# Kernel optimization log

Hardware: AMD Instinct MI355X
Metric: run time of the kernel (lower is better)

The kernel has to match this reference:

```python
import jax, jax.numpy as jnp
import numpy as np

N = 100000      # nodes
E = 1600000     # graph edges (avg degree 16)
Q = 1000000     # query edges to score
IN, HID, OUT = 128, 128, 64


def setup_inputs() -> dict:
    key = jax.random.key(0)
    ks = jax.random.split(key, 7)
    feat = jax.random.normal(ks[0], (N, IN), dtype=jnp.float32)
    edge_src = jax.random.randint(ks[1], (E,), 0, N, dtype=jnp.int32)
    edge_dst = jax.random.randint(ks[2], (E,), 0, N, dtype=jnp.int32)
    src = jax.random.randint(ks[3], (Q,), 0, N, dtype=jnp.int32)
    dst = jax.random.randint(ks[4], (Q,), 0, N, dtype=jnp.int32)
    W1 = jax.random.normal(ks[5], (IN, HID), dtype=jnp.float32) / np.sqrt(IN).astype(np.float32)
    b1 = jnp.zeros((HID,), jnp.float32)
    W2 = jax.random.normal(ks[6], (HID, OUT), dtype=jnp.float32) / np.sqrt(HID).astype(np.float32)
    b2 = jnp.zeros((OUT,), jnp.float32)
    return {"feat": feat, "edge_src": edge_src, "edge_dst": edge_dst,
            "src": src, "dst": dst, "W1": W1, "b1": b1, "W2": W2, "b2": b2}


def _graph_conv(h, W, b, edge_src, edge_dst, out_norm, in_norm):
    """DGL GraphConv(norm='both'): D_out^{-1/2} -> aggregate -> D_in^{-1/2}, W, b.
    DGL applies W before aggregation when in_feats > out_feats (same math)."""
    n = h.shape[0]
    h = h * out_norm[:, None]
    if h.shape[1] > W.shape[1]:
        h = h @ W
        agg = jax.ops.segment_sum(h[edge_src], edge_dst, num_segments=n)
    else:
        agg = jax.ops.segment_sum(h[edge_src], edge_dst, num_segments=n)
        agg = agg @ W
    return agg * in_norm[:, None] + b


def reference(feat, edge_src, edge_dst, src, dst, W1, b1, W2, b2):
    n = feat.shape[0]
    ones = jnp.ones((edge_src.shape[0],), feat.dtype)
    out_deg = jax.ops.segment_sum(ones, edge_src, num_segments=n)
    in_deg = jax.ops.segment_sum(ones, edge_dst, num_segments=n)
    out_norm = jnp.maximum(out_deg, 1.0) ** -0.5
    in_norm = jnp.maximum(in_deg, 1.0) ** -0.5

    h = _graph_conv(feat, W1, b1, edge_src, edge_dst, out_norm, in_norm)
    h = jax.nn.relu(h)  # dropout is identity at inference
    h = _graph_conv(h, W2, b2, edge_src, edge_dst, out_norm, in_norm)

    edge_scores = jnp.sum(h[src] * h[dst], axis=-1)
    return jax.nn.sigmoid(edge_scores)
```

## Files before the change

kernel.cpp:

```cpp
#include <hip/hip_runtime.h>
#include <math.h>

static inline size_t align256(size_t x) { return (x + 255) & ~(size_t)255; }

typedef __attribute__((ext_vector_type(8))) short bf16x8;
typedef __attribute__((ext_vector_type(4))) float f32x4;

__device__ inline float bfLo(unsigned int u) {
  union { unsigned int i; float f; } v; v.i = u << 16; return v.f;
}
__device__ inline float bfHi(unsigned int u) {
  union { unsigned int i; float f; } v; v.i = u & 0xffff0000u; return v.f;
}
__device__ inline float bf2f(unsigned short u) {
  union { unsigned int i; float f; } v; v.i = ((unsigned int)u) << 16; return v.f;
}
__device__ inline unsigned short f2bf(float f) {
  union { float f; unsigned int i; } v; v.f = f;
  unsigned int r = v.i + 0x7FFF + ((v.i >> 16) & 1);
  return (unsigned short)(r >> 16);
}
__device__ inline unsigned int packbf(float lo, float hi) {
  return ((unsigned int)f2bf(hi) << 16) | f2bf(lo);
}

__global__ __launch_bounds__(256) void k_coarse_count(const int* __restrict__ esrc,
                                                      const int* __restrict__ edst,
                                                      int E, int chunk, int NB, int G,
                                                      int* __restrict__ blkD,
                                                      int* __restrict__ blkS) {
  __shared__ int hD[512], hS[512];
  int blk = blockIdx.x, tid = threadIdx.x;
  for (int i = tid; i < NB; i += 256) { hD[i] = 0; hS[i] = 0; }
  __syncthreads();
  int s0 = blk * chunk, s1 = min(E, s0 + chunk);
  for (int e = s0 + tid; e < s1; e += 256) {
    atomicAdd(&hD[edst[e] >> 8], 1);
    atomicAdd(&hS[esrc[e] >> 8], 1);
  }
  __syncthreads();
  for (int i = tid; i < NB; i += 256) {
    blkD[i * G + blk] = hD[i];
    blkS[i * G + blk] = hS[i];
  }
}

__global__ __launch_bounds__(256) void k_scan1(const int* __restrict__ in,
                                               int* __restrict__ out,
                                               int* __restrict__ bsums, int n) {
  __shared__ int s[256];
  int tid = threadIdx.x, gid = blockIdx.x * 256 + tid;
  int v = (gid < n) ? in[gid] : 0;
  s[tid] = v; __syncthreads();
  for (int o = 1; o < 256; o <<= 1) {
    int t = (tid >= o) ? s[tid - o] : 0;
    __syncthreads();
    s[tid] += t;
    __syncthreads();
  }
  if (gid < n) out[gid] = s[tid] - v;
  if (tid == 255) bsums[blockIdx.x] = s[255];
}

__global__ __launch_bounds__(512) void k_scan2(int* __restrict__ bsums, int nb) {
  __shared__ int s[512];
  int tid = threadIdx.x;
  int* base = bsums + blockIdx.x * nb;
  int v = (tid < nb) ? base[tid] : 0;
  s[tid] = v; __syncthreads();
  for (int o = 1; o < 512; o <<= 1) {
    int t = (tid >= o) ? s[tid - o] : 0;
    __syncthreads();
    s[tid] += t;
    __syncthreads();
  }
  if (tid < nb) base[tid] = s[tid] - v;
}

__global__ __launch_bounds__(256) void k_scan3b(int* __restrict__ arr,
                                                const int* __restrict__ bsums, int n) {
  int gid = blockIdx.x * 256 + threadIdx.x;
  if (gid < n) arr[gid] += bsums[blockIdx.x];
}

__global__ __launch_bounds__(256) void k_coarse_scatter(const int* __restrict__ esrc,
                                                        const int* __restrict__ edst,
                                                        int E, int chunk, int NB, int G,
                                                        const int* __restrict__ scD,
                                                        const int* __restrict__ scS,
                                                        unsigned int* __restrict__ pairs,
                                                        unsigned int* __restrict__ keys) {
  __shared__ int cD[512], cS[512];
  int blk = blockIdx.x, tid = threadIdx.x;
  for (int i = tid; i < NB; i += 256) {
    cD[i] = scD[i * G + blk];
    cS[i] = scS[i * G + blk];
  }
  __syncthreads();
  int s0 = blk * chunk, s1 = min(E, s0 + chunk);
  for (int e = s0 + tid; e < s1; e += 256) {
    int s = esrc[e], d = edst[e];
    int pd = atomicAdd(&cD[d >> 8], 1);
    pairs[pd] = ((unsigned)s << 8) | ((unsigned)d & 255u);
    int ps = atomicAdd(&cS[s >> 8], 1);
    keys[ps] = (unsigned)s;
  }
}

__global__ __launch_bounds__(256) void k_fine(const unsigned int* __restrict__ pairs,
                                              const unsigned int* __restrict__ keys,
                                              const int* __restrict__ scD,
                                              const int* __restrict__ scS,
                                              int G, int E, int N, int NB,
                                              int* __restrict__ cntIn,
                                              float* __restrict__ normIn,
                                              int* __restrict__ offs,
                                              int* __restrict__ csr,
                                              float* __restrict__ normOut) {
  __shared__ int hist[256], scn[256], cur[256];
  int tid = threadIdx.x;
  if (blockIdx.x >= (unsigned)NB) {
    int b = blockIdx.x - NB;
    int bstart = scS[b * G];
    int bend = (b + 1 < NB) ? scS[(b + 1) * G] : E;
    hist[tid] = 0;
    __syncthreads();
    for (int e = bstart + tid; e < bend; e += 256)
      atomicAdd(&hist[keys[e] & 255u], 1);
    __syncthreads();
    int node = b * 256 + tid;
    if (node < N) normOut[node] = rsqrtf((float)max(hist[tid], 1));
    return;
  }
  int b = blockIdx.x;
  int bstart = scD[b * G];
  int bend = (b + 1 < NB) ? scD[(b + 1) * G] : E;
  hist[tid] = 0;
  __syncthreads();
  for (int e = bstart + tid; e < bend; e += 256)
    atomicAdd(&hist[pairs[e] & 255u], 1);
  __syncthreads();
  int v = hist[tid];
  scn[tid] = v;
  __syncthreads();
  for (int o = 1; o < 256; o <<= 1) {
    int t = (tid >= o) ? scn[tid - o] : 0;
    __syncthreads();
    scn[tid] += t;
    __syncthreads();
  }
  int excl = scn[tid] - v;
  cur[tid] = excl;
  int node = b * 256 + tid;
  if (node < N) {
    cntIn[node] = v;
    normIn[node] = rsqrtf((float)max(v, 1));
    offs[node] = bstart + excl;
  }
  __syncthreads();
  for (int e = bstart + tid; e < bend; e += 256) {
    unsigned int u = pairs[e];
    int p = bstart + atomicAdd(&cur[u & 255u], 1);
    csr[p] = (int)(u >> 8);
  }
}

__global__ __launch_bounds__(256) void k_prep(const float* __restrict__ W1,
                                              const float* __restrict__ W2,
                                              unsigned short* __restrict__ W1t,
                                              unsigned short* __restrict__ W2t) {
  int t = blockIdx.x * 256 + threadIdx.x;
  int stride = gridDim.x * 256;
  for (int i = t; i < 128 * 128; i += stride) {
    int nn = i >> 7, kk = i & 127;
    W1t[i] = f2bf(W1[kk * 128 + nn]);
  }
  for (int i = t; i < 64 * 128; i += stride) {
    int nn = i >> 7, kk = i & 127;
    W2t[i] = f2bf(W2[kk * 64 + nn]);
  }
}

template <int C, typename TA>
__global__ __launch_bounds__(256) void k_mgemm(const TA* __restrict__ A,
                                               const float* __restrict__ scale,
                                               const unsigned short* __restrict__ Wt,
                                               unsigned short* __restrict__ out, int n) {
  constexpr int KP = 136;
  constexpr int NCH = C / 16;
  __shared__ __align__(16) unsigned short Al[64 * KP];
  __shared__ __align__(16) unsigned short Wl[C * KP];
  int tid = threadIdx.x;
  int r0 = blockIdx.x * 64;

  {
    const uint4* Wg = (const uint4*)Wt;
    uint4* Wd = (uint4*)Wl;
    for (int idx = tid; idx < C * 16; idx += 256) {
      int row = idx >> 4, seg = idx & 15;
      Wd[row * 17 + seg] = Wg[idx];
    }
  }
  {
    int seg = tid & 7;
    for (int it = 0; it < 2; ++it) {
      int row = (tid >> 3) + it * 32;
      int g = r0 + row;
      float v[16];
      if (g < n) {
        float sc = scale[g];
        if constexpr (sizeof(TA) == 4) {
          const float4* Ag = (const float4*)((const float*)A + (size_t)g * 128);
#pragma unroll
          for (int j = 0; j < 4; ++j) {
            float4 f = Ag[seg * 4 + j];
            v[j * 4 + 0] = f.x * sc; v[j * 4 + 1] = f.y * sc;
            v[j * 4 + 2] = f.z * sc; v[j * 4 + 3] = f.w * sc;
          }
        } else {
          const uint4* Ag = (const uint4*)((const unsigned short*)A + (size_t)g * 128);
#pragma unroll
          for (int j = 0; j < 2; ++j) {
            uint4 u = Ag[seg * 2 + j];
            v[j * 8 + 0] = bfLo(u.x) * sc; v[j * 8 + 1] = bfHi(u.x) * sc;
            v[j * 8 + 2] = bfLo(u.y) * sc; v[j * 8 + 3] = bfHi(u.y) * sc;
            v[j * 8 + 4] = bfLo(u.z) * sc; v[j * 8 + 5] = bfHi(u.z) * sc;
            v[j * 8 + 6] = bfLo(u.w) * sc; v[j * 8 + 7] = bfHi(u.w) * sc;
          }
        }
      } else {
#pragma unroll
        for (int j = 0; j < 16; ++j) v[j] = 0.f;
      }
      uint4* dst = (uint4*)(Al + row * KP + seg * 16);
      dst[0] = make_uint4(packbf(v[0], v[1]), packbf(v[2], v[3]),
                          packbf(v[4], v[5]), packbf(v[6], v[7]));
      dst[1] = make_uint4(packbf(v[8], v[9]), packbf(v[10], v[11]),
                          packbf(v[12], v[13]), packbf(v[14], v[15]));
    }
  }
  __syncthreads();

  int lane = tid & 63;
  int w = tid >> 6;
  int quad = lane >> 4, m16 = lane & 15;
  f32x4 acc[NCH];
#pragma unroll
  for (int c = 0; c < NCH; ++c) acc[c] = (f32x4){0.f, 0.f, 0.f, 0.f};

#pragma unroll
  for (int kc = 0; kc < 4; ++kc) {
    int ko = kc * 32 + quad * 8;
    bf16x8 a = *(const bf16x8*)(Al + (w * 16 + m16) * KP + ko);
#pragma unroll
    for (int c = 0; c < NCH; ++c) {
      bf16x8 b = *(const bf16x8*)(Wl + (c * 16 + m16) * KP + ko);
      acc[c] = __builtin_amdgcn_mfma_f32_16x16x32_bf16(a, b, acc[c], 0, 0, 0);
    }
  }

#pragma unroll
  for (int c = 0; c < NCH; ++c)
#pragma unroll
    for (int r = 0; r < 4; ++r) {
      int g = r0 + w * 16 + quad * 4 + r;
      if (g < n) out[(size_t)g * C + c * 16 + m16] = f2bf(acc[c][r]);
    }
}

__global__ __launch_bounds__(256) void k_agg128_relu(const unsigned short* __restrict__ X,
                                                     const int* __restrict__ csr,
                                                     const int* __restrict__ offs,
                                                     const int* __restrict__ cnt,
                                                     const float* __restrict__ norm,
                                                     const float* __restrict__ bias,
                                                     unsigned short* __restrict__ H, int n) {
  int wid = blockIdx.x * 4 + (threadIdx.x >> 6);
  if (wid >= n) return;
  int lane = threadIdx.x & 63;
  int sub = lane & 15;
  int grp = lane >> 4;
  int start = offs[wid], m = cnt[wid];
  const int* p = csr + start;
  const uint4* Xv = (const uint4*)X;
  float a[8] = {0.f, 0.f, 0.f, 0.f, 0.f, 0.f, 0.f, 0.f};
  for (int c0 = 0; c0 < m; c0 += 64) {
    int take = min(64, m - c0);
    int iv = p[c0 + ((lane < take) ? lane : take - 1)];
    int e = 0;
    for (; e + 16 <= take; e += 16) {
      uint4 uu[4];
#pragma unroll
      for (int j = 0; j < 4; ++j) {
        int ss = __shfl(iv, e + j * 4 + grp);
        uu[j] = Xv[(size_t)ss * 16 + sub];
      }
#pragma unroll
      for (int j = 0; j < 4; ++j) {
        a[0] += bfLo(uu[j].x); a[1] += bfHi(uu[j].x);
        a[2] += bfLo(uu[j].y); a[3] += bfHi(uu[j].y);
        a[4] += bfLo(uu[j].z); a[5] += bfHi(uu[j].z);
        a[6] += bfLo(uu[j].w); a[7] += bfHi(uu[j].w);
      }
    }
    for (; e + 4 <= take; e += 4) {
      int ss = __shfl(iv, e + grp);
      uint4 u = Xv[(size_t)ss * 16 + sub];
      a[0] += bfLo(u.x); a[1] += bfHi(u.x);
      a[2] += bfLo(u.y); a[3] += bfHi(u.y);
      a[4] += bfLo(u.z); a[5] += bfHi(u.z);
      a[6] += bfLo(u.w); a[7] += bfHi(u.w);
    }
    int r = take - e;
    if (r > 0) {
      int ss = __shfl(iv, min(e + grp, take - 1));
      uint4 u = Xv[(size_t)ss * 16 + sub];
      if (grp < r) {
        a[0] += bfLo(u.x); a[1] += bfHi(u.x);
        a[2] += bfLo(u.y); a[3] += bfHi(u.y);
        a[4] += bfLo(u.z); a[5] += bfHi(u.z);
        a[6] += bfLo(u.w); a[7] += bfHi(u.w);
      }
    }
  }
#pragma unroll
  for (int k = 0; k < 8; ++k) {
    a[k] += __shfl_xor(a[k], 16);
    a[k] += __shfl_xor(a[k], 32);
  }
  float nm = norm[wid];
  const float4* bv = (const float4*)bias;
  float4 b0 = bv[sub * 2], b1 = bv[sub * 2 + 1];
  if (grp == 0) {
    float o0 = fmaxf(a[0] * nm + b0.x, 0.f);
    float o1 = fmaxf(a[1] * nm + b0.y, 0.f);
    float o2 = fmaxf(a[2] * nm + b0.z, 0.f);
    float o3 = fmaxf(a[3] * nm + b0.w, 0.f);
    float o4 = fmaxf(a[4] * nm + b1.x, 0.f);
    float o5 = fmaxf(a[5] * nm + b1.y, 0.f);
    float o6 = fmaxf(a[6] * nm + b1.z, 0.f);
    float o7 = fmaxf(a[7] * nm + b1.w, 0.f);
    uint4 o = make_uint4(packbf(o0, o1), packbf(o2, o3),
                         packbf(o4, o5), packbf(o6, o7));
    ((uint4*)H)[(size_t)wid * 16 + sub] = o;
  }
}

__global__ __launch_bounds__(256) void k_agg64(const unsigned short* __restrict__ X,
                                               const int* __restrict__ csr,
                                               const int* __restrict__ offs,
                                               const int* __restrict__ cnt,
                                               const float* __restrict__ norm,
                                               const float* __restrict__ bias,
                                               unsigned short* __restrict__ H, int n) {
  int wid = blockIdx.x * 4 + (threadIdx.x >> 6);
  if (wid >= n) return;
  int lane = threadIdx.x & 63;
  int sub = lane & 7;
  int grp = lane >> 3;
  int start = offs[wid], m = cnt[wid];
  const int* p = csr + start;
  const uint4* Xv = (const uint4*)X;
  float a[8] = {0.f, 0.f, 0.f, 0.f, 0.f, 0.f, 0.f, 0.f};
  for (int c0 = 0; c0 < m; c0 += 64) {
    int take = min(64, m - c0);
    int iv = p[c0 + ((lane < take) ? lane : take - 1)];
    int e = 0;
    for (; e + 16 <= take; e += 16) {
      uint4 uu[2];
#pragma unroll
      for (int j = 0; j < 2; ++j) {
        int ss = __shfl(iv, e + j * 8 + grp);
        uu[j] = Xv[(size_t)ss * 8 + sub];
      }
#pragma unroll
      for (int j = 0; j < 2; ++j) {
        a[0] += bfLo(uu[j].x); a[1] += bfHi(uu[j].x);
        a[2] += bfLo(uu[j].y); a[3] += bfHi(uu[j].y);
        a[4] += bfLo(uu[j].z); a[5] += bfHi(uu[j].z);
        a[6] += bfLo(uu[j].w); a[7] += bfHi(uu[j].w);
      }
    }
    for (; e + 8 <= take; e += 8) {
      int ss = __shfl(iv, e + grp);
      uint4 u = Xv[(size_t)ss * 8 + sub];
      a[0] += bfLo(u.x); a[1] += bfHi(u.x);
      a[2] += bfLo(u.y); a[3] += bfHi(u.y);
      a[4] += bfLo(u.z); a[5] += bfHi(u.z);
      a[6] += bfLo(u.w); a[7] += bfHi(u.w);
    }
    int r = take - e;
    if (r > 0) {
      int ss = __shfl(iv, min(e + grp, take - 1));
      uint4 u = Xv[(size_t)ss * 8 + sub];
      if (grp < r) {
        a[0] += bfLo(u.x); a[1] += bfHi(u.x);
        a[2] += bfLo(u.y); a[3] += bfHi(u.y);
        a[4] += bfLo(u.z); a[5] += bfHi(u.z);
        a[6] += bfLo(u.w); a[7] += bfHi(u.w);
      }
    }
  }
#pragma unroll
  for (int k = 0; k < 8; ++k) {
    a[k] += __shfl_xor(a[k], 8);
    a[k] += __shfl_xor(a[k], 16);
    a[k] += __shfl_xor(a[k], 32);
  }
  float nm = norm[wid];
  const float4* bv = (const float4*)bias;
  float4 b0 = bv[sub * 2], b1 = bv[sub * 2 + 1];
  if (grp == 0) {
    uint4 o = make_uint4(packbf(a[0] * nm + b0.x, a[1] * nm + b0.y),
                         packbf(a[2] * nm + b0.z, a[3] * nm + b0.w),
                         packbf(a[4] * nm + b1.x, a[5] * nm + b1.y),
                         packbf(a[6] * nm + b1.z, a[7] * nm + b1.w));
    ((uint4*)H)[(size_t)wid * 8 + sub] = o;
  }
}

__global__ __launch_bounds__(256) void k_score(const unsigned short* __restrict__ H,
                                               const int* __restrict__ qs,
                                               const int* __restrict__ qd,
                                               float* __restrict__ out, int q) {
  int t = blockIdx.x * 256 + threadIdx.x;
  int sub = t & 7;
  int q0 = t >> 3;
  float p = 0.f;
  if (q0 < q) {
    int s = qs[q0], d = qd[q0];
    const uint4* Hv = (const uint4*)H;
    uint4 a = Hv[(size_t)s * 8 + sub];
    uint4 b = Hv[(size_t)d * 8 + sub];
    p = bfLo(a.x) * bfLo(b.x) + bfHi(a.x) * bfHi(b.x) +
        bfLo(a.y) * bfLo(b.y) + bfHi(a.y) * bfHi(b.y) +
        bfLo(a.z) * bfLo(b.z) + bfHi(a.z) * bfHi(b.z) +
        bfLo(a.w) * bfLo(b.w) + bfHi(a.w) * bfHi(b.w);
  }
  p += __shfl_xor(p, 1);
  p += __shfl_xor(p, 2);
  p += __shfl_xor(p, 4);
  if (sub == 0 && q0 < q) out[q0] = 1.f / (1.f + expf(-p));
}

extern "C" void kernel_launch(void* const* d_in, const int* in_sizes, int n_in,
                              void* d_out, int out_size, void* d_ws, size_t ws_size,
                              hipStream_t stream) {
  const float* feat = (const float*)d_in[0];
  const int* esrc   = (const int*)d_in[1];
  const int* edst   = (const int*)d_in[2];
  const int* qsrc   = (const int*)d_in[3];
  const int* qdst   = (const int*)d_in[4];
  const float* W1   = (const float*)d_in[5];
  const float* b1   = (const float*)d_in[6];
  const float* W2   = (const float*)d_in[7];
  const float* b2   = (const float*)d_in[8];
  float* out = (float*)d_out;

  const int N = in_sizes[0] / 128;
  const int E = in_sizes[1];
  const int Q = in_sizes[3];

  const int G = 256;
  const int NB = (N + 255) >> 8;
  const int chunk = (E + G - 1) / G;
  const int lenS = NB * G;
  const int gScan = lenS / 256;

  char* w = (char*)d_ws;
  size_t o = 0;
  unsigned short* X1 = (unsigned short*)(w + o); o += align256((size_t)N * 128 * 2);
  unsigned short* X2 = (unsigned short*)(w + o); o += align256((size_t)N * 64 * 2);
  unsigned short* H2 = (unsigned short*)(w + o); o += align256((size_t)N * 64 * 2);
  int* cntIn = (int*)(w + o);       o += align256((size_t)N * 4);
  float* normOut = (float*)(w + o); o += align256((size_t)N * 4);
  float* normIn = (float*)(w + o);  o += align256((size_t)N * 4);
  int* offs = (int*)(w + o);        o += align256((size_t)N * 4);
  int* blk = (int*)(w + o);         o += align256((size_t)lenS * 8);
  int* sc = (int*)(w + o);          o += align256((size_t)lenS * 8);
  int* bsums = (int*)(w + o);       o += align256((size_t)8192);
  unsigned short* W1t = (unsigned short*)(w + o); o += align256((size_t)128 * 128 * 2);
  unsigned short* W2t = (unsigned short*)(w + o); o += align256((size_t)64 * 128 * 2);
  unsigned int* pairs = (unsigned int*)(w + o); o += align256((size_t)E * 4);
  unsigned int* keys = (unsigned int*)(w + o); o += align256((size_t)E * 4);
  int* csr = (int*)(w + o);         o += align256((size_t)E * 4);

  int* blkD = blk;        int* blkS = blk + lenS;
  int* scD = sc;          int* scS = sc + lenS;

  k_prep<<<64, 256, 0, stream>>>(W1, W2, W1t, W2t);

  k_coarse_count<<<G, 256, 0, stream>>>(esrc, edst, E, chunk, NB, G, blkD, blkS);
  k_scan1<<<2 * gScan, 256, 0, stream>>>(blk, sc, bsums, 2 * lenS);
  k_scan2<<<2, 512, 0, stream>>>(bsums, gScan);
  k_scan3b<<<2 * gScan, 256, 0, stream>>>(sc, bsums, 2 * lenS);
  k_coarse_scatter<<<G, 256, 0, stream>>>(esrc, edst, E, chunk, NB, G, scD, scS, pairs, keys);
  k_fine<<<2 * NB, 256, 0, stream>>>(pairs, keys, scD, scS, G, E, N, NB,
                                     cntIn, normIn, offs, csr, normOut);

  const int gRows = (N + 63) / 64;
  k_mgemm<128, float><<<gRows, 256, 0, stream>>>(feat, normOut, W1t, X1, N);
  k_agg128_relu<<<(N + 3) / 4, 256, 0, stream>>>(X1, csr, offs, cntIn, normIn, b1, X2, N);
  k_mgemm<64, unsigned short><<<gRows, 256, 0, stream>>>(X2, normOut, W2t, X1, N);
  k_agg64<<<(N + 3) / 4, 256, 0, stream>>>(X1, csr, offs, cntIn, normIn, b2, H2, N);
  k_score<<<((Q * 8) + 255) / 256, 256, 0, stream>>>(H2, qsrc, qdst, out, Q);
}
```

Baseline: 325.3 us.

## Fold weight prep and scan fixup into neighbours; split layer-1 aggregation by XCD halves

Weight transpose/convert moves into the coarse-count kernel, and the scan block-offset add is folded into the scatter and fine kernels. This removes two launches and one pass over the scan array. Layer-1 aggregation now splits each node's 128 features into two 64-feature halves processed by different blocks. Blocks are remapped so each half lands on a fixed group of four XCDs, which is meant to improve L2 locality of the gathered rows. Unroll depth in both aggregation loops doubles to keep more gathers in flight. The cost is duplicated CSR index reads and twice as many waves for layer 1.

```diff
diff --git a/kernel.cpp b/kernel.cpp
--- a/kernel.cpp
+++ b/kernel.cpp
@@ -28,9 +28,22 @@
                                                       const int* __restrict__ edst,
                                                       int E, int chunk, int NB, int G,
                                                       int* __restrict__ blkD,
-                                                      int* __restrict__ blkS) {
+                                                      int* __restrict__ blkS,
+                                                      const float* __restrict__ W1,
+                                                      const float* __restrict__ W2,
+                                                      unsigned short* __restrict__ W1t,
+                                                      unsigned short* __restrict__ W2t) {
   __shared__ int hD[512], hS[512];
   int blk = blockIdx.x, tid = threadIdx.x;
+  int t = blk * 256 + tid;
+  if (t < 128 * 128) {
+    int nn = t >> 7, kk = t & 127;
+    W1t[t] = f2bf(W1[kk * 128 + nn]);
+  }
+  if (t < 64 * 128) {
+    int nn = t >> 7, kk = t & 127;
+    W2t[t] = f2bf(W2[kk * 64 + nn]);
+  }
   for (int i = tid; i < NB; i += 256) { hD[i] = 0; hS[i] = 0; }
   __syncthreads();
   int s0 = blk * chunk, s1 = min(E, s0 + chunk);
@@ -77,24 +90,19 @@
   if (tid < nb) base[tid] = s[tid] - v;
 }
 
-__global__ __launch_bounds__(256) void k_scan3b(int* __restrict__ arr,
-                                                const int* __restrict__ bsums, int n) {
-  int gid = blockIdx.x * 256 + threadIdx.x;
-  if (gid < n) arr[gid] += bsums[blockIdx.x];
-}
-
 __global__ __launch_bounds__(256) void k_coarse_scatter(const int* __restrict__ esrc,
                                                         const int* __restrict__ edst,
                                                         int E, int chunk, int NB, int G,
                                                         const int* __restrict__ scD,
                                                         const int* __restrict__ scS,
+                                                        const int* __restrict__ bsums,
                                                         unsigned int* __restrict__ pairs,
                                                         unsigned int* __restrict__ keys) {
   __shared__ int cD[512], cS[512];
   int blk = blockIdx.x, tid = threadIdx.x;
   for (int i = tid; i < NB; i += 256) {
-    cD[i] = scD[i * G + blk];
-    cS[i] = scS[i * G + blk];
+    cD[i] = scD[i * G + blk] + bsums[i];
+    cS[i] = scS[i * G + blk] + bsums[NB + i];
   }
   __syncthreads();
   int s0 = blk * chunk, s1 = min(E, s0 + chunk);
@@ -111,6 +119,7 @@
                                               const unsigned int* __restrict__ keys,
                                               const int* __restrict__ scD,
                                               const int* __restrict__ scS,
+                                              const int* __restrict__ bsums,
                                               int G, int E, int N, int NB,
                                               int* __restrict__ cntIn,
                                               float* __restrict__ normIn,
@@ -121,8 +130,8 @@
   int tid = threadIdx.x;
   if (blockIdx.x >= (unsigned)NB) {
     int b = blockIdx.x - NB;
-    int bstart = scS[b * G];
-    int bend = (b + 1 < NB) ? scS[(b + 1) * G] : E;
+    int bstart = scS[b * G] + bsums[NB + b];
+    int bend = (b + 1 < NB) ? scS[(b + 1) * G] + bsums[NB + b + 1] : E;
     hist[tid] = 0;
     __syncthreads();
     for (int e = bstart + tid; e < bend; e += 256)
@@ -133,8 +142,8 @@
     return;
   }
   int b = blockIdx.x;
-  int bstart = scD[b * G];
-  int bend = (b + 1 < NB) ? scD[(b + 1) * G] : E;
+  int bstart = scD[b * G] + bsums[b];
+  int bend = (b + 1 < NB) ? scD[(b + 1) * G] + bsums[b + 1] : E;
   hist[tid] = 0;
   __syncthreads();
   for (int e = bstart + tid; e < bend; e += 256)
@@ -162,22 +171,6 @@
     unsigned int u = pairs[e];
     int p = bstart + atomicAdd(&cur[u & 255u], 1);
     csr[p] = (int)(u >> 8);
-  }
-}
-
-__global__ __launch_bounds__(256) void k_prep(const float* __restrict__ W1,
-                                              const float* __restrict__ W2,
-                                              unsigned short* __restrict__ W1t,
-                                              unsigned short* __restrict__ W2t) {
-  int t = blockIdx.x * 256 + threadIdx.x;
-  int stride = gridDim.x * 256;
-  for (int i = t; i < 128 * 128; i += stride) {
-    int nn = i >> 7, kk = i & 127;
-    W1t[i] = f2bf(W1[kk * 128 + nn]);
-  }
-  for (int i = t; i < 64 * 128; i += stride) {
-    int nn = i >> 7, kk = i & 127;
-    W2t[i] = f2bf(W2[kk * 64 + nn]);
   }
 }
 
@@ -268,18 +261,23 @@
     }
 }
 
-__global__ __launch_bounds__(256) void k_agg128_relu(const unsigned short* __restrict__ X,
-                                                     const int* __restrict__ csr,
-                                                     const int* __restrict__ offs,
-                                                     const int* __restrict__ cnt,
-                                                     const float* __restrict__ norm,
-                                                     const float* __restrict__ bias,
-                                                     unsigned short* __restrict__ H, int n) {
-  int wid = blockIdx.x * 4 + (threadIdx.x >> 6);
+__global__ __launch_bounds__(256) void k_agg128h(const unsigned short* __restrict__ X,
+                                                 const int* __restrict__ csr,
+                                                 const int* __restrict__ offs,
+                                                 const int* __restrict__ cnt,
+                                                 const float* __restrict__ norm,
+                                                 const float* __restrict__ bias,
+                                                 unsigned short* __restrict__ H, int n) {
+  int b = blockIdx.x;
+  int xcd = b & 7;
+  int half = xcd >> 2;
+  int grpIdx = (b >> 3) * 4 + (xcd & 3);
+  int wid = grpIdx * 4 + (threadIdx.x >> 6);
   if (wid >= n) return;
   int lane = threadIdx.x & 63;
-  int sub = lane & 15;
-  int grp = lane >> 4;
+  int sub = lane & 7;
+  int grp = lane >> 3;
+  int hoff = half * 8;
   int start = offs[wid], m = cnt[wid];
   const int* p = csr + start;
   const uint4* Xv = (const uint4*)X;
@@ -288,12 +286,12 @@
     int take = min(64, m - c0);
     int iv = p[c0 + ((lane < take) ? lane : take - 1)];
     int e = 0;
-    for (; e + 16 <= take; e += 16) {
+    for (; e + 32 <= take; e += 32) {
       uint4 uu[4];
 #pragma unroll
       for (int j = 0; j < 4; ++j) {
-        int ss = __shfl(iv, e + j * 4 + grp);
-        uu[j] = Xv[(size_t)ss * 16 + sub];
+        int ss = __shfl(iv, e + j * 8 + grp);
+        uu[j] = Xv[(size_t)ss * 16 + hoff + sub];
       }
 #pragma unroll
       for (int j = 0; j < 4; ++j) {
@@ -303,9 +301,9 @@
         a[6] += bfLo(uu[j].w); a[7] += bfHi(uu[j].w);
       }
     }
-    for (; e + 4 <= take; e += 4) {
+    for (; e + 8 <= take; e += 8) {
       int ss = __shfl(iv, e + grp);
-      uint4 u = Xv[(size_t)ss * 16 + sub];
+      uint4 u = Xv[(size_t)ss * 16 + hoff + sub];
       a[0] += bfLo(u.x); a[1] += bfHi(u.x);
       a[2] += bfLo(u.y); a[3] += bfHi(u.y);
       a[4] += bfLo(u.z); a[5] += bfHi(u.z);
@@ -314,7 +312,7 @@
     int r = take - e;
     if (r > 0) {
       int ss = __shfl(iv, min(e + grp, take - 1));
-      uint4 u = Xv[(size_t)ss * 16 + sub];
+      uint4 u = Xv[(size_t)ss * 16 + hoff + sub];
       if (grp < r) {
         a[0] += bfLo(u.x); a[1] += bfHi(u.x);
         a[2] += bfLo(u.y); a[3] += bfHi(u.y);
@@ -325,12 +323,13 @@
   }
 #pragma unroll
   for (int k = 0; k < 8; ++k) {
+    a[k] += __shfl_xor(a[k], 8);
     a[k] += __shfl_xor(a[k], 16);
     a[k] += __shfl_xor(a[k], 32);
   }
   float nm = norm[wid];
   const float4* bv = (const float4*)bias;
-  float4 b0 = bv[sub * 2], b1 = bv[sub * 2 + 1];
+  float4 b0 = bv[half * 16 + sub * 2], b1 = bv[half * 16 + sub * 2 + 1];
   if (grp == 0) {
     float o0 = fmaxf(a[0] * nm + b0.x, 0.f);
     float o1 = fmaxf(a[1] * nm + b0.y, 0.f);
@@ -342,7 +341,7 @@
     float o7 = fmaxf(a[7] * nm + b1.w, 0.f);
     uint4 o = make_uint4(packbf(o0, o1), packbf(o2, o3),
                          packbf(o4, o5), packbf(o6, o7));
-    ((uint4*)H)[(size_t)wid * 16 + sub] = o;
+    ((uint4*)H)[(size_t)wid * 16 + hoff + sub] = o;
   }
 }
 
@@ -366,15 +365,15 @@
     int take = min(64, m - c0);
     int iv = p[c0 + ((lane < take) ? lane : take - 1)];
     int e = 0;
-    for (; e + 16 <= take; e += 16) {
-      uint4 uu[2];
-#pragma unroll
-      for (int j = 0; j < 2; ++j) {
+    for (; e + 32 <= take; e += 32) {
+      uint4 uu[4];
+#pragma unroll
+      for (int j = 0; j < 4; ++j) {
         int ss = __shfl(iv, e + j * 8 + grp);
         uu[j] = Xv[(size_t)ss * 8 + sub];
       }
 #pragma unroll
-      for (int j = 0; j < 2; ++j) {
+      for (int j = 0; j < 4; ++j) {
         a[0] += bfLo(uu[j].x); a[1] += bfHi(uu[j].x);
         a[2] += bfLo(uu[j].y); a[3] += bfHi(uu[j].y);
         a[4] += bfLo(uu[j].z); a[5] += bfHi(uu[j].z);
@@ -488,19 +487,20 @@
   int* blkD = blk;        int* blkS = blk + lenS;
   int* scD = sc;          int* scS = sc + lenS;
 
-  k_prep<<<64, 256, 0, stream>>>(W1, W2, W1t, W2t);
-
-  k_coarse_count<<<G, 256, 0, stream>>>(esrc, edst, E, chunk, NB, G, blkD, blkS);
+  k_coarse_count<<<G, 256, 0, stream>>>(esrc, edst, E, chunk, NB, G, blkD, blkS,
+                                        W1, W2, W1t, W2t);
   k_scan1<<<2 * gScan, 256, 0, stream>>>(blk, sc, bsums, 2 * lenS);
   k_scan2<<<2, 512, 0, stream>>>(bsums, gScan);
-  k_scan3b<<<2 * gScan, 256, 0, stream>>>(sc, bsums, 2 * lenS);
-  k_coarse_scatter<<<G, 256, 0, stream>>>(esrc, edst, E, chunk, NB, G, scD, scS, pairs, keys);
-  k_fine<<<2 * NB, 256, 0, stream>>>(pairs, keys, scD, scS, G, E, N, NB,
+  k_coarse_scatter<<<G, 256, 0, stream>>>(esrc, edst, E, chunk, NB, G, scD, scS,
+                                          bsums, pairs, keys);
+  k_fine<<<2 * NB, 256, 0, stream>>>(pairs, keys, scD, scS, bsums, G, E, N, NB,
                                      cntIn, normIn, offs, csr, normOut);
 
   const int gRows = (N + 63) / 64;
+  const int nGrp4 = (N + 3) / 4;
+  const int gAggH = 8 * ((nGrp4 + 3) / 4);
   k_mgemm<128, float><<<gRows, 256, 0, stream>>>(feat, normOut, W1t, X1, N);
-  k_agg128_relu<<<(N + 3) / 4, 256, 0, stream>>>(X1, csr, offs, cntIn, normIn, b1, X2, N);
+  k_agg128h<<<gAggH, 256, 0, stream>>>(X1, csr, offs, cntIn, normIn, b1, X2, N);
   k_mgemm<64, unsigned short><<<gRows, 256, 0, stream>>>(X2, normOut, W2t, X1, N);
   k_agg64<<<(N + 3) / 4, 256, 0, stream>>>(X1, csr, offs, cntIn, normIn, b2, H2, N);
   k_score<<<((Q * 8) + 255) / 256, 256, 0, stream>>>(H2, qsrc, qdst, out, Q);
```

Result: slower. 353.0 us (+8.5%).
